# Kernel optimization log

Measured on AMD Instinct MI355X. Metric: run time of the kernel, lower is better.

The kernel has to match this reference:

```python
import jax, jax.numpy as jnp
import numpy as np

SUB_NO, T_NO, T_DATA, E_NO, I_NO, N_BASIS = 20, 200, 50000, 2000, 500, 20


def _make_cos_basis():
    x = np.arange(T_NO, dtype=np.float32)
    raw = 6.0 * np.log(x + 1.0)  # cos_scale=6, cos_shift=1
    basis = np.zeros((N_BASIS, T_NO), np.float32)
    for i in range(N_BASIS):
        phi = 0.5 * np.pi * i
        b = 0.5 * np.cos(raw - phi) + 0.5
        basis[i] = np.where((raw < phi - np.pi) | (raw > phi + np.pi), 0.0, b)
    return basis


def _make_tree():
    C = np.zeros((SUB_NO, SUB_NO), np.int32)
    for p in range(SUB_NO):
        for c in (2 * p + 1, 2 * p + 2):
            if c < SUB_NO:
                C[p, c] = 1
    return C


def _one_hot_assign(n_syn):
    C = np.zeros((SUB_NO, n_syn), np.int32)
    C[np.arange(n_syn) % SUB_NO, np.arange(n_syn)] = 1
    return C


def setup_inputs() -> dict:
    key = jax.random.key(0)
    ks = jax.random.split(key, 12)
    f32 = jnp.float32
    S_e = (jax.random.uniform(ks[0], (T_DATA, E_NO)) < 0.02).astype(f32)
    S_i = (jax.random.uniform(ks[1], (T_DATA, I_NO)) < 0.02).astype(f32)
    Z = (jax.random.uniform(ks[2], (T_DATA,)) < 0.05).astype(f32)
    return {
        "S_e": S_e, "S_i": S_i, "Z": Z,
        "C_den": jnp.asarray(_make_tree()),
        "C_syn_e": jnp.asarray(_one_hot_assign(E_NO)),
        "C_syn_i": jnp.asarray(_one_hot_assign(I_NO)),
        "cos_basis": jnp.asarray(_make_cos_basis()),
        "W_syn": jax.random.normal(ks[3], (SUB_NO, N_BASIS, 2), f32) * 0.1,
        "W_hist": jax.random.normal(ks[4], (N_BASIS,), f32) * 0.1,
        "W_sub": jnp.ones((SUB_NO,), f32) * 0.1,
        "W_spk": jnp.ones((1,), f32),
        "Tau_spk": jnp.ones((1,), f32) * 3.0,
        "V_o": jax.random.normal(ks[5], (1,), f32),
        "Theta": jax.random.normal(ks[6], (SUB_NO,), f32) * 0.1,
        "weight1": jax.random.normal(ks[7], (SUB_NO, 5), f32) * 0.1,
        "weight2": jax.random.normal(ks[8], (SUB_NO, 5, 5), f32) * 0.1,
        "weight3": jax.random.normal(ks[9], (SUB_NO, 5, 5), f32) * 0.1,
        "weight4": jax.random.normal(ks[10], (5, SUB_NO), f32) * 0.1,
    }


def reference(S_e, S_i, Z, C_den, C_syn_e, C_syn_i, cos_basis, W_syn, W_hist,
              W_sub, W_spk, Tau_spk, V_o, Theta, weight1, weight2, weight3, weight4):
    f32 = jnp.float32
    T = S_e.shape[0]
    sub_no = weight1.shape[0]
    T_no = cos_basis.shape[1]
    Cd = C_den.astype(f32)

    # synapse -> subunit projection
    syn_e = S_e @ C_syn_e.astype(f32).T  # [T, sub]
    syn_i = S_i @ C_syn_i.astype(f32).T

    e_kern = W_syn[:, :, 0] @ cos_basis  # [sub, T_no]
    i_kern = W_syn[:, :, 1] @ cos_basis

    def grouped_causal_conv(x, kern):
        # torch: pad T_no-1 zeros in front, grouped conv with flipped kernel (true causal conv)
        xp = jnp.pad(x, ((T_no - 1, 0), (0, 0))).T[None]  # [1, sub, T+T_no-1]
        k = kern[:, None, ::-1]  # [sub, 1, T_no]
        y = jax.lax.conv_general_dilated(xp, k, (1,), 'VALID',
                                         dimension_numbers=('NCH', 'OIH', 'NCH'),
                                         feature_group_count=x.shape[1])
        return y[0].T  # [T, sub]

    syn = grouped_causal_conv(syn_e, e_kern) + grouped_causal_conv(syn_i, i_kern)

    def causal_conv_lag1(z, kern):
        # torch: pad T_no zeros in front, valid conv with flipped kernel, drop last -> [T]
        zp = jnp.pad(z, (T_no, 0))[None, None]  # [1,1,T+T_no]
        k = kern[None, None, ::-1]
        y = jax.lax.conv_general_dilated(zp, k, (1,), 'VALID',
                                         dimension_numbers=('NCH', 'OIH', 'NCH'))
        return y[0, 0, :-1]

    hist_kern = W_hist @ cos_basis  # [T_no]
    hist_filt = causal_conv_lag1(Z, hist_kern)

    lrelu = jax.nn.leaky_relu  # negative_slope 0.01 matches torch default
    W_sub2 = W_sub ** 2

    def sub_mlp(s, x):
        h = lrelu(x[:, None] * weight1[s][None, :])  # [T,5]
        h = lrelu(h @ weight2[s])
        h = lrelu(h @ weight3[s])
        return h @ weight4[:, s]  # [T]

    # tree recurrence: children have higher index, processed last-to-first
    ns_out = jnp.zeros((T, sub_no), f32)
    for s in range(sub_no - 1):
        sub_idx = sub_no - 1 - s
        agg = ns_out @ (Cd[sub_idx] * W_sub2)  # equals gather-leaf weighted sum (0 if leaf)
        ns_in = lrelu(syn[:, sub_idx] + Theta[sub_idx] + agg)
        ns_out = ns_out.at[:, sub_idx].set(sub_mlp(sub_idx, ns_in))

    root_in = lrelu(hist_filt + syn[:, 0] + ns_out @ (Cd[0] * W_sub2) + Theta[0])
    final_Z = jax.nn.sigmoid(sub_mlp(0, root_in))

    t = jnp.arange(T_no, dtype=f32)
    t_tau = t / Tau_spk[0] ** 2
    spk_kern = t_tau * jnp.exp(-t_tau) * W_spk[0] ** 2
    final_V = causal_conv_lag1(Z, spk_kern) + V_o[0]

    out_filters = jnp.concatenate([e_kern, i_kern, hist_kern[None, :]], axis=0)
    return final_V, final_Z, out_filters
```

## Files before the change

### kernel.cpp

```cpp
#include <hip/hip_runtime.h>
#include <math.h>

#define T_DATA 50000
#define SUB_NO 20
#define T_NO 200
#define N_BASIS 20

#define WS_E    0
#define WS_I    1000000
#define WS_EKT  2000000
#define WS_IKT  2004000
#define WS_WSE  2008400
#define WS_HF   2008800

#define KA_RED_BLOCKS 977
#define KA_HIST_BLOCKS 196
#define KA_TOTAL (KA_RED_BLOCKS + 1 + KA_HIST_BLOCKS)

__device__ __forceinline__ float lrelu(float x) { return x > 0.f ? x : 0.01f * x; }

__global__ __launch_bounds__(256) void kA(const float* __restrict__ Se,
                                          const float* __restrict__ Si,
                                          const float* __restrict__ Z,
                                          const int* __restrict__ C_den,
                                          const float* __restrict__ cb,
                                          const float* __restrict__ W_syn,
                                          const float* __restrict__ W_hist,
                                          const float* __restrict__ W_sub,
                                          const float* __restrict__ W_spk,
                                          const float* __restrict__ Tau,
                                          const float* __restrict__ Vo,
                                          float* __restrict__ ws,
                                          float* __restrict__ out) {
    int tid = threadIdx.x;
    int bid = blockIdx.x;

    if (bid < KA_RED_BLOCKS) {
        int gid = bid * 256 + tid;
        if (gid >= T_DATA * 5) return;
        int t = gid / 5, sg = gid % 5;
        const float4* Se4 = (const float4*)Se;
        const float4* Si4 = (const float4*)Si;

        float4 a = make_float4(0.f, 0.f, 0.f, 0.f);
        int base_e = t * 500 + sg;
        #pragma unroll 10
        for (int g = 0; g < 100; g++) {
            float4 v = Se4[base_e + g * 5];
            a.x += v.x; a.y += v.y; a.z += v.z; a.w += v.w;
        }
        float4 b = make_float4(0.f, 0.f, 0.f, 0.f);
        int base_i = t * 125 + sg;
        #pragma unroll
        for (int g = 0; g < 25; g++) {
            float4 v = Si4[base_i + g * 5];
            b.x += v.x; b.y += v.y; b.z += v.z; b.w += v.w;
        }
        ((float4*)(ws + WS_E))[t * 5 + sg] = a;
        ((float4*)(ws + WS_I))[t * 5 + sg] = b;
        return;
    }

    if (bid == KA_RED_BLOCKS) {
        for (int j = tid; j < 4000; j += 256) {
            int s = j / 200, tau = j % 200;
            float se = 0.f, si = 0.f;
            #pragma unroll
            for (int b = 0; b < N_BASIS; b++) {
                float c = cb[b * 200 + tau];
                se += W_syn[(s * N_BASIS + b) * 2 + 0] * c;
                si += W_syn[(s * N_BASIS + b) * 2 + 1] * c;
            }
            ws[WS_EKT + tau * 20 + s] = se;
            ws[WS_IKT + tau * 20 + s] = si;
            out[2 * T_DATA + j] = se;
            out[2 * T_DATA + 4000 + j] = si;
        }
        for (int j = tid; j < 200; j += 256) {
            float h = 0.f;
            #pragma unroll
            for (int b = 0; b < N_BASIS; b++) h += W_hist[b] * cb[b * 200 + j];
            out[2 * T_DATA + 8000 + j] = h;
        }
        for (int j = tid; j < 400; j += 256) {
            int c = j % 20;
            ws[WS_WSE + j] = (float)C_den[j] * W_sub[c] * W_sub[c];
        }
        return;
    }

    __shared__ float z[456];
    __shared__ float2 hk[200];
    int t0 = (bid - KA_RED_BLOCKS - 1) * 256;
    for (int f = tid; f < 456; f += 256) {
        int u = t0 - 200 + f;
        z[f] = (u >= 0 && u < T_DATA) ? Z[u] : 0.f;
    }
    if (tid < 200) {
        float h = 0.f;
        #pragma unroll
        for (int b = 0; b < N_BASIS; b++) h += W_hist[b] * cb[b * 200 + tid];
        float tau2 = Tau[0] * Tau[0];
        float tt = (float)tid / tau2;
        float sk = tt * expf(-tt) * W_spk[0] * W_spk[0];
        hk[tid] = make_float2(h, sk);
    }
    __syncthreads();
    float ha = 0.f, sa = 0.f;
    #pragma unroll 4
    for (int tau = 0; tau < T_NO; tau++) {
        float zv = z[tid + 199 - tau];
        float2 hv = hk[tau];
        ha += zv * hv.x;
        sa += zv * hv.y;
    }
    int t = t0 + tid;
    if (t < T_DATA) {
        out[t] = sa + Vo[0];
        ws[WS_HF + t] = ha;
    }
}

__device__ __forceinline__ float sub_mlp(int s, float x,
                                         const float* __restrict__ w1,
                                         const float* __restrict__ w2,
                                         const float* __restrict__ w3,
                                         const float* __restrict__ w4) {
    float h1[5], h2[5], h3[5];
    #pragma unroll
    for (int k = 0; k < 5; k++) h1[k] = lrelu(x * w1[s * 5 + k]);
    #pragma unroll
    for (int j = 0; j < 5; j++) {
        float v = 0.f;
        #pragma unroll
        for (int k = 0; k < 5; k++) v += h1[k] * w2[s * 25 + k * 5 + j];
        h2[j] = lrelu(v);
    }
    #pragma unroll
    for (int j = 0; j < 5; j++) {
        float v = 0.f;
        #pragma unroll
        for (int k = 0; k < 5; k++) v += h2[k] * w3[s * 25 + k * 5 + j];
        h3[j] = lrelu(v);
    }
    float o = 0.f;
    #pragma unroll
    for (int k = 0; k < 5; k++) o += h3[k] * w4[k * 20 + s];
    return o;
}

#define KB_X 64
#define KB_T 256
#define KB_ROWS 455
#define KB_SRP 115
#define KB_THREADS 640

__global__ __launch_bounds__(KB_THREADS) void kB(const float* __restrict__ ws,
                                                 const float* __restrict__ Theta,
                                                 const float* __restrict__ w1,
                                                 const float* __restrict__ w2,
                                                 const float* __restrict__ w3,
                                                 const float* __restrict__ w4,
                                                 float* __restrict__ out) {
    __shared__ float4 tile[2 * 5 * 4 * KB_SRP];
    __shared__ float4 hkE[1000];
    __shared__ float4 hkI[1000];
    int x = threadIdx.x;
    int sg = __builtin_amdgcn_readfirstlane(threadIdx.y);
    int z  = __builtin_amdgcn_readfirstlane(threadIdx.z);
    int t0 = blockIdx.x * KB_T;
    int lin = x + 64 * sg + 320 * z;

    const float4* wsE4 = (const float4*)(ws + WS_E);
    const float4* wsI4 = (const float4*)(ws + WS_I);
    long gbase = (long)(t0 - 199) * 5;
    for (int f = lin; f < KB_ROWS * 5; f += KB_THREADS) {
        long g = gbase + f;
        int row = f / 5, gg = f % 5;
        int sub = row & 3, idx = row >> 2;
        float4 ve = make_float4(0.f, 0.f, 0.f, 0.f);
        float4 vi = ve;
        if (g >= 0 && g < (long)T_DATA * 5) {
            ve = wsE4[g];
            vi = wsI4[g];
        }
        tile[((0 * 5 + gg) * 4 + sub) * KB_SRP + idx] = ve;
        tile[((1 * 5 + gg) * 4 + sub) * KB_SRP + idx] = vi;
    }
    const float4* eK = (const float4*)(ws + WS_EKT);
    const float4* iK = (const float4*)(ws + WS_IKT);
    for (int f = lin; f < 1000; f += KB_THREADS) {
        hkE[f] = eK[f];
        hkI[f] = iK[f];
    }
    __syncthreads();

    const float4* te = &tile[(0 * 5 + sg) * 4 * KB_SRP];
    const float4* ti = &tile[(1 * 5 + sg) * 4 * KB_SRP];

    float4 we[4], wi[4], acc[4];
    #pragma unroll
    for (int j = 0; j < 4; j++) acc[j] = make_float4(0.f, 0.f, 0.f, 0.f);
    int idx0 = x + 50 - 25 * z;
    we[0] = te[0 * KB_SRP + idx0]; wi[0] = ti[0 * KB_SRP + idx0];
    we[1] = te[1 * KB_SRP + idx0]; wi[1] = ti[1 * KB_SRP + idx0];
    we[2] = te[2 * KB_SRP + idx0]; wi[2] = ti[2 * KB_SRP + idx0];

    int m0 = 25 * z;
    for (int mm = 0; mm < 25; mm++) {
        int m = m0 + mm;
        int idx = x + 49 - m;
        #pragma unroll
        for (int p = 0; p < 4; p++) {
            int tau = 4 * m + p;
            const int s0 = (3 - p) & 3;
            we[s0] = te[s0 * KB_SRP + idx];
            wi[s0] = ti[s0 * KB_SRP + idx];
            float4 ke = hkE[tau * 5 + sg];
            float4 ki = hkI[tau * 5 + sg];
            #pragma unroll
            for (int j = 0; j < 4; j++) {
                const int sl = (s0 + j) & 3;
                acc[j].x += we[sl].x * ke.x + wi[sl].x * ki.x;
                acc[j].y += we[sl].y * ke.y + wi[sl].y * ki.y;
                acc[j].z += we[sl].z * ke.z + wi[sl].z * ki.z;
                acc[j].w += we[sl].w * ke.w + wi[sl].w * ki.w;
            }
        }
    }

    __syncthreads();
    float4* accP = tile;
    #pragma unroll
    for (int j = 0; j < 4; j++) accP[((z * 20) + sg * 4 + j) * 64 + x] = acc[j];
    __syncthreads();

    if (lin >= 256) return;
    int w = lin >> 6, xr = lin & 63;
    int t = t0 + 4 * xr + w;
    if (t >= T_DATA) return;

    float acc20[20];
    #pragma unroll
    for (int g = 0; g < 5; g++) {
        float4 v0 = accP[(g * 4 + w) * 64 + xr];
        float4 v1 = accP[(20 + g * 4 + w) * 64 + xr];
        acc20[g * 4 + 0] = v0.x + v1.x; acc20[g * 4 + 1] = v0.y + v1.y;
        acc20[g * 4 + 2] = v0.z + v1.z; acc20[g * 4 + 3] = v0.w + v1.w;
    }
    const float* wse = ws + WS_WSE;
    float ns[20];
    #pragma unroll
    for (int s = 0; s < 20; s++) ns[s] = 0.f;
    #pragma unroll
    for (int si = 19; si >= 1; si--) {
        float ag = 0.f;
        #pragma unroll
        for (int c = 0; c < 20; c++) ag += wse[si * 20 + c] * ns[c];
        float xx = lrelu(acc20[si] + Theta[si] + ag);
        ns[si] = sub_mlp(si, xx, w1, w2, w3, w4);
    }
    float ag0 = 0.f;
    #pragma unroll
    for (int c = 0; c < 20; c++) ag0 += wse[c] * ns[c];
    float x0 = lrelu(ws[WS_HF + t] + acc20[0] + ag0 + Theta[0]);
    float zf = sub_mlp(0, x0, w1, w2, w3, w4);
    out[T_DATA + t] = 1.f / (1.f + expf(-zf));
}

extern "C" void kernel_launch(void* const* d_in, const int* in_sizes, int n_in,
                              void* d_out, int out_size, void* d_ws, size_t ws_size,
                              hipStream_t stream) {
    const float* S_e    = (const float*)d_in[0];
    const float* S_i    = (const float*)d_in[1];
    const float* Z      = (const float*)d_in[2];
    const int*   C_den  = (const int*)d_in[3];
    const float* cb     = (const float*)d_in[6];
    const float* W_syn  = (const float*)d_in[7];
    const float* W_hist = (const float*)d_in[8];
    const float* W_sub  = (const float*)d_in[9];
    const float* W_spk  = (const float*)d_in[10];
    const float* Tau    = (const float*)d_in[11];
    const float* V_o    = (const float*)d_in[12];
    const float* Theta  = (const float*)d_in[13];
    const float* w1     = (const float*)d_in[14];
    const float* w2     = (const float*)d_in[15];
    const float* w3     = (const float*)d_in[16];
    const float* w4     = (const float*)d_in[17];
    float* out = (float*)d_out;
    float* ws  = (float*)d_ws;

    kA<<<KA_TOTAL, 256, 0, stream>>>(S_e, S_i, Z, C_den, cb, W_syn, W_hist,
                                     W_sub, W_spk, Tau, V_o, ws, out);
    dim3 b3(KB_X, 5, 2);
    kB<<<(T_DATA + KB_T - 1) / KB_T, b3, 0, stream>>>(
        ws, Theta, w1, w2, w3, w4, out);
}
```

Before: 657.4 us.

## Restructure spike reduction for contiguous loads and read kernels from global in kB

The reduction phase of kA now runs 320 threads per block covering 64 time rows. Each thread reads a contiguous 100-float4 chunk of a row (25 for S_i) into five strided partial sums, and a shared-memory pass then combines the partials across the five thread groups into the same grouped output layout. This is meant to make the bandwidth-bound scan of S_e and S_i more cache-line friendly. In kB, the filter kernels are no longer staged in LDS and are read straight from global memory in the inner loop. That saves LDS and allows more blocks per CU, at the risk of more global or cache traffic in the hot loop.

```diff
diff --git a/kernel.cpp b/kernel.cpp
--- a/kernel.cpp
+++ b/kernel.cpp
@@ -13,56 +13,102 @@
 #define WS_WSE  2008400
 #define WS_HF   2008800
 
-#define KA_RED_BLOCKS 977
-#define KA_HIST_BLOCKS 196
+#define KA_THREADS 320
+#define KA_RED_BLOCKS 782
+#define KA_HIST_BLOCKS 157
 #define KA_TOTAL (KA_RED_BLOCKS + 1 + KA_HIST_BLOCKS)
 
 __device__ __forceinline__ float lrelu(float x) { return x > 0.f ? x : 0.01f * x; }
 
-__global__ __launch_bounds__(256) void kA(const float* __restrict__ Se,
-                                          const float* __restrict__ Si,
-                                          const float* __restrict__ Z,
-                                          const int* __restrict__ C_den,
-                                          const float* __restrict__ cb,
-                                          const float* __restrict__ W_syn,
-                                          const float* __restrict__ W_hist,
-                                          const float* __restrict__ W_sub,
-                                          const float* __restrict__ W_spk,
-                                          const float* __restrict__ Tau,
-                                          const float* __restrict__ Vo,
-                                          float* __restrict__ ws,
-                                          float* __restrict__ out) {
+__global__ __launch_bounds__(KA_THREADS) void kA(const float* __restrict__ Se,
+                                                 const float* __restrict__ Si,
+                                                 const float* __restrict__ Z,
+                                                 const int* __restrict__ C_den,
+                                                 const float* __restrict__ cb,
+                                                 const float* __restrict__ W_syn,
+                                                 const float* __restrict__ W_hist,
+                                                 const float* __restrict__ W_sub,
+                                                 const float* __restrict__ W_spk,
+                                                 const float* __restrict__ Tau,
+                                                 const float* __restrict__ Vo,
+                                                 float* __restrict__ ws,
+                                                 float* __restrict__ out) {
     int tid = threadIdx.x;
     int bid = blockIdx.x;
 
+    __shared__ float4 red[KA_THREADS * 5];
+    __shared__ float zsh[520];
+    __shared__ float2 hk[200];
+
     if (bid < KA_RED_BLOCKS) {
-        int gid = bid * 256 + tid;
-        if (gid >= T_DATA * 5) return;
-        int t = gid / 5, sg = gid % 5;
+        int r2 = tid / 5, sg = tid % 5;
+        int t = bid * 64 + r2;
+        bool valid = (t < T_DATA);
         const float4* Se4 = (const float4*)Se;
         const float4* Si4 = (const float4*)Si;
 
-        float4 a = make_float4(0.f, 0.f, 0.f, 0.f);
-        int base_e = t * 500 + sg;
-        #pragma unroll 10
-        for (int g = 0; g < 100; g++) {
-            float4 v = Se4[base_e + g * 5];
-            a.x += v.x; a.y += v.y; a.z += v.z; a.w += v.w;
-        }
-        float4 b = make_float4(0.f, 0.f, 0.f, 0.f);
-        int base_i = t * 125 + sg;
-        #pragma unroll
-        for (int g = 0; g < 25; g++) {
-            float4 v = Si4[base_i + g * 5];
-            b.x += v.x; b.y += v.y; b.z += v.z; b.w += v.w;
-        }
-        ((float4*)(ws + WS_E))[t * 5 + sg] = a;
-        ((float4*)(ws + WS_I))[t * 5 + sg] = b;
+        float4 aE[5], aI[5];
+        #pragma unroll
+        for (int r = 0; r < 5; r++) {
+            aE[r] = make_float4(0.f, 0.f, 0.f, 0.f);
+            aI[r] = aE[r];
+        }
+        if (valid) {
+            const float4* rowE = Se4 + (long)t * 500 + sg * 100;
+            #pragma unroll 2
+            for (int uu = 0; uu < 20; uu++) {
+                #pragma unroll
+                for (int r = 0; r < 5; r++) {
+                    float4 v = rowE[uu * 5 + r];
+                    aE[r].x += v.x; aE[r].y += v.y;
+                    aE[r].z += v.z; aE[r].w += v.w;
+                }
+            }
+            const float4* rowI = Si4 + (long)t * 125 + sg * 25;
+            #pragma unroll 2
+            for (int uu = 0; uu < 5; uu++) {
+                #pragma unroll
+                for (int r = 0; r < 5; r++) {
+                    float4 v = rowI[uu * 5 + r];
+                    aI[r].x += v.x; aI[r].y += v.y;
+                    aI[r].z += v.z; aI[r].w += v.w;
+                }
+            }
+        }
+        #pragma unroll
+        for (int r = 0; r < 5; r++) red[tid * 5 + r] = aE[r];
+        __syncthreads();
+        {
+            int rr = tid / 5, k = tid % 5;
+            float4 s = make_float4(0.f, 0.f, 0.f, 0.f);
+            #pragma unroll
+            for (int g = 0; g < 5; g++) {
+                float4 v = red[(rr * 5 + g) * 5 + k];
+                s.x += v.x; s.y += v.y; s.z += v.z; s.w += v.w;
+            }
+            if (t < T_DATA)
+                ((float4*)(ws + WS_E))[bid * KA_THREADS + tid] = s;
+        }
+        __syncthreads();
+        #pragma unroll
+        for (int r = 0; r < 5; r++) red[tid * 5 + r] = aI[r];
+        __syncthreads();
+        {
+            int rr = tid / 5, k = tid % 5;
+            float4 s = make_float4(0.f, 0.f, 0.f, 0.f);
+            #pragma unroll
+            for (int g = 0; g < 5; g++) {
+                float4 v = red[(rr * 5 + g) * 5 + k];
+                s.x += v.x; s.y += v.y; s.z += v.z; s.w += v.w;
+            }
+            if (t < T_DATA)
+                ((float4*)(ws + WS_I))[bid * KA_THREADS + tid] = s;
+        }
         return;
     }
 
     if (bid == KA_RED_BLOCKS) {
-        for (int j = tid; j < 4000; j += 256) {
+        for (int j = tid; j < 4000; j += KA_THREADS) {
             int s = j / 200, tau = j % 200;
             float se = 0.f, si = 0.f;
             #pragma unroll
@@ -76,25 +122,23 @@
             out[2 * T_DATA + j] = se;
             out[2 * T_DATA + 4000 + j] = si;
         }
-        for (int j = tid; j < 200; j += 256) {
+        for (int j = tid; j < 200; j += KA_THREADS) {
             float h = 0.f;
             #pragma unroll
             for (int b = 0; b < N_BASIS; b++) h += W_hist[b] * cb[b * 200 + j];
             out[2 * T_DATA + 8000 + j] = h;
         }
-        for (int j = tid; j < 400; j += 256) {
+        for (int j = tid; j < 400; j += KA_THREADS) {
             int c = j % 20;
             ws[WS_WSE + j] = (float)C_den[j] * W_sub[c] * W_sub[c];
         }
         return;
     }
 
-    __shared__ float z[456];
-    __shared__ float2 hk[200];
-    int t0 = (bid - KA_RED_BLOCKS - 1) * 256;
-    for (int f = tid; f < 456; f += 256) {
+    int t0 = (bid - KA_RED_BLOCKS - 1) * KA_THREADS;
+    for (int f = tid; f < 520; f += KA_THREADS) {
         int u = t0 - 200 + f;
-        z[f] = (u >= 0 && u < T_DATA) ? Z[u] : 0.f;
+        zsh[f] = (u >= 0 && u < T_DATA) ? Z[u] : 0.f;
     }
     if (tid < 200) {
         float h = 0.f;
@@ -109,7 +153,7 @@
     float ha = 0.f, sa = 0.f;
     #pragma unroll 4
     for (int tau = 0; tau < T_NO; tau++) {
-        float zv = z[tid + 199 - tau];
+        float zv = zsh[tid + 199 - tau];
         float2 hv = hk[tau];
         ha += zv * hv.x;
         sa += zv * hv.y;
@@ -163,8 +207,6 @@
                                                  const float* __restrict__ w4,
                                                  float* __restrict__ out) {
     __shared__ float4 tile[2 * 5 * 4 * KB_SRP];
-    __shared__ float4 hkE[1000];
-    __shared__ float4 hkI[1000];
     int x = threadIdx.x;
     int sg = __builtin_amdgcn_readfirstlane(threadIdx.y);
     int z  = __builtin_amdgcn_readfirstlane(threadIdx.z);
@@ -187,14 +229,10 @@
         tile[((0 * 5 + gg) * 4 + sub) * KB_SRP + idx] = ve;
         tile[((1 * 5 + gg) * 4 + sub) * KB_SRP + idx] = vi;
     }
+    __syncthreads();
+
     const float4* eK = (const float4*)(ws + WS_EKT);
     const float4* iK = (const float4*)(ws + WS_IKT);
-    for (int f = lin; f < 1000; f += KB_THREADS) {
-        hkE[f] = eK[f];
-        hkI[f] = iK[f];
-    }
-    __syncthreads();
-
     const float4* te = &tile[(0 * 5 + sg) * 4 * KB_SRP];
     const float4* ti = &tile[(1 * 5 + sg) * 4 * KB_SRP];
 
@@ -216,8 +254,8 @@
             const int s0 = (3 - p) & 3;
             we[s0] = te[s0 * KB_SRP + idx];
             wi[s0] = ti[s0 * KB_SRP + idx];
-            float4 ke = hkE[tau * 5 + sg];
-            float4 ki = hkI[tau * 5 + sg];
+            float4 ke = eK[tau * 5 + sg];
+            float4 ki = iK[tau * 5 + sg];
             #pragma unroll
             for (int j = 0; j < 4; j++) {
                 const int sl = (s0 + j) & 3;
@@ -290,8 +328,9 @@
     float* out = (float*)d_out;
     float* ws  = (float*)d_ws;
 
-    kA<<<KA_TOTAL, 256, 0, stream>>>(S_e, S_i, Z, C_den, cb, W_syn, W_hist,
-                                     W_sub, W_spk, Tau, V_o, ws, out);
+    kA<<<KA_TOTAL, KA_THREADS, 0, stream>>>(S_e, S_i, Z, C_den, cb, W_syn,
+                                            W_hist, W_sub, W_spk, Tau, V_o,
+                                            ws, out);
     dim3 b3(KB_X, 5, 2);
     kB<<<(T_DATA + KB_T - 1) / KB_T, b3, 0, stream>>>(
         ws, Theta, w1, w2, w3, w4, out);
```

New measurement: 695.3 us. 5.8% more time.

## Fuse both kernels into one cooperative persistent kernel with grid sync

Applied to the files above, without the earlier changes.

Merges the reduction/filter kernel and the convolution+tree kernel into a single cooperative launch of 256 blocks. A grid-wide barrier separates the two phases, removing one kernel launch and its gap. The history convolution now reads Z straight from global memory instead of staging it in shared memory. The convolution kernels are also read from global memory instead of being copied into LDS. Risks include grid-sync overhead, and the reduction phase now running on only 256 blocks, which may give less memory parallelism than the earlier 977 blocks.

```diff
diff --git a/kernel.cpp b/kernel.cpp
--- a/kernel.cpp
+++ b/kernel.cpp
@@ -1,8 +1,10 @@
 #include <hip/hip_runtime.h>
+#include <hip/hip_cooperative_groups.h>
 #include <math.h>
 
+namespace cg = cooperative_groups;
+
 #define T_DATA 50000
-#define SUB_NO 20
 #define T_NO 200
 #define N_BASIS 20
 
@@ -13,113 +15,16 @@
 #define WS_WSE  2008400
 #define WS_HF   2008800
 
-#define KA_RED_BLOCKS 977
-#define KA_HIST_BLOCKS 196
-#define KA_TOTAL (KA_RED_BLOCKS + 1 + KA_HIST_BLOCKS)
+#define NBLK 256
+#define NTHR 640
+#define GSTRIDE (NBLK * NTHR)
+
+#define KB_T 256
+#define KB_ROWS 455
+#define KB_SRP 115
+#define KB_CHUNKS 196
 
 __device__ __forceinline__ float lrelu(float x) { return x > 0.f ? x : 0.01f * x; }
-
-__global__ __launch_bounds__(256) void kA(const float* __restrict__ Se,
-                                          const float* __restrict__ Si,
-                                          const float* __restrict__ Z,
-                                          const int* __restrict__ C_den,
-                                          const float* __restrict__ cb,
-                                          const float* __restrict__ W_syn,
-                                          const float* __restrict__ W_hist,
-                                          const float* __restrict__ W_sub,
-                                          const float* __restrict__ W_spk,
-                                          const float* __restrict__ Tau,
-                                          const float* __restrict__ Vo,
-                                          float* __restrict__ ws,
-                                          float* __restrict__ out) {
-    int tid = threadIdx.x;
-    int bid = blockIdx.x;
-
-    if (bid < KA_RED_BLOCKS) {
-        int gid = bid * 256 + tid;
-        if (gid >= T_DATA * 5) return;
-        int t = gid / 5, sg = gid % 5;
-        const float4* Se4 = (const float4*)Se;
-        const float4* Si4 = (const float4*)Si;
-
-        float4 a = make_float4(0.f, 0.f, 0.f, 0.f);
-        int base_e = t * 500 + sg;
-        #pragma unroll 10
-        for (int g = 0; g < 100; g++) {
-            float4 v = Se4[base_e + g * 5];
-            a.x += v.x; a.y += v.y; a.z += v.z; a.w += v.w;
-        }
-        float4 b = make_float4(0.f, 0.f, 0.f, 0.f);
-        int base_i = t * 125 + sg;
-        #pragma unroll
-        for (int g = 0; g < 25; g++) {
-            float4 v = Si4[base_i + g * 5];
-            b.x += v.x; b.y += v.y; b.z += v.z; b.w += v.w;
-        }
-        ((float4*)(ws + WS_E))[t * 5 + sg] = a;
-        ((float4*)(ws + WS_I))[t * 5 + sg] = b;
-        return;
-    }
-
-    if (bid == KA_RED_BLOCKS) {
-        for (int j = tid; j < 4000; j += 256) {
-            int s = j / 200, tau = j % 200;
-            float se = 0.f, si = 0.f;
-            #pragma unroll
-            for (int b = 0; b < N_BASIS; b++) {
-                float c = cb[b * 200 + tau];
-                se += W_syn[(s * N_BASIS + b) * 2 + 0] * c;
-                si += W_syn[(s * N_BASIS + b) * 2 + 1] * c;
-            }
-            ws[WS_EKT + tau * 20 + s] = se;
-            ws[WS_IKT + tau * 20 + s] = si;
-            out[2 * T_DATA + j] = se;
-            out[2 * T_DATA + 4000 + j] = si;
-        }
-        for (int j = tid; j < 200; j += 256) {
-            float h = 0.f;
-            #pragma unroll
-            for (int b = 0; b < N_BASIS; b++) h += W_hist[b] * cb[b * 200 + j];
-            out[2 * T_DATA + 8000 + j] = h;
-        }
-        for (int j = tid; j < 400; j += 256) {
-            int c = j % 20;
-            ws[WS_WSE + j] = (float)C_den[j] * W_sub[c] * W_sub[c];
-        }
-        return;
-    }
-
-    __shared__ float z[456];
-    __shared__ float2 hk[200];
-    int t0 = (bid - KA_RED_BLOCKS - 1) * 256;
-    for (int f = tid; f < 456; f += 256) {
-        int u = t0 - 200 + f;
-        z[f] = (u >= 0 && u < T_DATA) ? Z[u] : 0.f;
-    }
-    if (tid < 200) {
-        float h = 0.f;
-        #pragma unroll
-        for (int b = 0; b < N_BASIS; b++) h += W_hist[b] * cb[b * 200 + tid];
-        float tau2 = Tau[0] * Tau[0];
-        float tt = (float)tid / tau2;
-        float sk = tt * expf(-tt) * W_spk[0] * W_spk[0];
-        hk[tid] = make_float2(h, sk);
-    }
-    __syncthreads();
-    float ha = 0.f, sa = 0.f;
-    #pragma unroll 4
-    for (int tau = 0; tau < T_NO; tau++) {
-        float zv = z[tid + 199 - tau];
-        float2 hv = hk[tau];
-        ha += zv * hv.x;
-        sa += zv * hv.y;
-    }
-    int t = t0 + tid;
-    if (t < T_DATA) {
-        out[t] = sa + Vo[0];
-        ws[WS_HF + t] = ha;
-    }
-}
 
 __device__ __forceinline__ float sub_mlp(int s, float x,
                                          const float* __restrict__ w1,
@@ -149,32 +54,118 @@
     return o;
 }
 
-#define KB_X 64
-#define KB_T 256
-#define KB_ROWS 455
-#define KB_SRP 115
-#define KB_THREADS 640
-
-__global__ __launch_bounds__(KB_THREADS) void kB(const float* __restrict__ ws,
-                                                 const float* __restrict__ Theta,
-                                                 const float* __restrict__ w1,
-                                                 const float* __restrict__ w2,
-                                                 const float* __restrict__ w3,
-                                                 const float* __restrict__ w4,
-                                                 float* __restrict__ out) {
-    __shared__ float4 tile[2 * 5 * 4 * KB_SRP];
-    __shared__ float4 hkE[1000];
-    __shared__ float4 hkI[1000];
-    int x = threadIdx.x;
-    int sg = __builtin_amdgcn_readfirstlane(threadIdx.y);
-    int z  = __builtin_amdgcn_readfirstlane(threadIdx.z);
-    int t0 = blockIdx.x * KB_T;
-    int lin = x + 64 * sg + 320 * z;
+__global__ __launch_bounds__(NTHR) void kFused(
+        const float* __restrict__ Se, const float* __restrict__ Si,
+        const float* __restrict__ Z, const int* __restrict__ C_den,
+        const float* __restrict__ cb, const float* __restrict__ W_syn,
+        const float* __restrict__ W_hist, const float* __restrict__ W_sub,
+        const float* __restrict__ W_spk, const float* __restrict__ Tau,
+        const float* __restrict__ Vo, const float* __restrict__ Theta,
+        const float* __restrict__ w1, const float* __restrict__ w2,
+        const float* __restrict__ w3, const float* __restrict__ w4,
+        float* __restrict__ ws, float* __restrict__ out) {
+    __shared__ float4 smem4[2 * 5 * 4 * KB_SRP];
+    int tid = threadIdx.x;
+    int bid = blockIdx.x;
+
+    {
+        const float4* Se4 = (const float4*)Se;
+        const float4* Si4 = (const float4*)Si;
+        float4* wsE4 = (float4*)(ws + WS_E);
+        float4* wsI4 = (float4*)(ws + WS_I);
+        for (int g = bid * NTHR + tid; g < T_DATA * 5; g += GSTRIDE) {
+            int t = g / 5, s5 = g % 5;
+            float4 a = make_float4(0.f, 0.f, 0.f, 0.f);
+            int base_e = t * 500 + s5;
+            #pragma unroll 10
+            for (int k = 0; k < 100; k++) {
+                float4 v = Se4[base_e + k * 5];
+                a.x += v.x; a.y += v.y; a.z += v.z; a.w += v.w;
+            }
+            float4 b = make_float4(0.f, 0.f, 0.f, 0.f);
+            int base_i = t * 125 + s5;
+            #pragma unroll
+            for (int k = 0; k < 25; k++) {
+                float4 v = Si4[base_i + k * 5];
+                b.x += v.x; b.y += v.y; b.z += v.z; b.w += v.w;
+            }
+            wsE4[g] = a;
+            wsI4[g] = b;
+        }
+    }
+
+    if (bid < 79) {
+        float2* hk = (float2*)smem4;
+        if (tid < 200) {
+            float h = 0.f;
+            #pragma unroll
+            for (int b = 0; b < N_BASIS; b++) h += W_hist[b] * cb[b * 200 + tid];
+            float tau2 = Tau[0] * Tau[0];
+            float tt = (float)tid / tau2;
+            float sk = tt * expf(-tt) * W_spk[0] * W_spk[0];
+            hk[tid] = make_float2(h, sk);
+        }
+        __syncthreads();
+        int t = bid * NTHR + tid;
+        if (t < T_DATA) {
+            float ha = 0.f, sa = 0.f;
+            #pragma unroll 4
+            for (int tau = 0; tau < T_NO; tau++) {
+                int u = t - 1 - tau;
+                float zv = (u >= 0) ? Z[u] : 0.f;
+                float2 hv = hk[tau];
+                ha += zv * hv.x;
+                sa += zv * hv.y;
+            }
+            out[t] = sa + Vo[0];
+            ws[WS_HF + t] = ha;
+        }
+    }
+
+    if (bid == NBLK - 1) {
+        for (int j = tid; j < 4000; j += NTHR) {
+            int s = j / 200, tau = j % 200;
+            float se = 0.f, si = 0.f;
+            #pragma unroll
+            for (int b = 0; b < N_BASIS; b++) {
+                float c = cb[b * 200 + tau];
+                se += W_syn[(s * N_BASIS + b) * 2 + 0] * c;
+                si += W_syn[(s * N_BASIS + b) * 2 + 1] * c;
+            }
+            ws[WS_EKT + tau * 20 + s] = se;
+            ws[WS_IKT + tau * 20 + s] = si;
+            out[2 * T_DATA + j] = se;
+            out[2 * T_DATA + 4000 + j] = si;
+        }
+        for (int j = tid; j < 200; j += NTHR) {
+            float h = 0.f;
+            #pragma unroll
+            for (int b = 0; b < N_BASIS; b++) h += W_hist[b] * cb[b * 200 + j];
+            out[2 * T_DATA + 8000 + j] = h;
+        }
+        for (int j = tid; j < 400; j += NTHR) {
+            int c = j % 20;
+            ws[WS_WSE + j] = (float)C_den[j] * W_sub[c] * W_sub[c];
+        }
+    }
+
+    __threadfence();
+    cg::this_grid().sync();
+
+    if (bid >= KB_CHUNKS) return;
+
+    float4* tile = smem4;
+    int x = tid & 63;
+    int wv = tid >> 6;
+    int sg = __builtin_amdgcn_readfirstlane(wv % 5);
+    int z  = __builtin_amdgcn_readfirstlane(wv / 5);
+    int t0 = bid * KB_T;
+    int lin = tid;
 
     const float4* wsE4 = (const float4*)(ws + WS_E);
     const float4* wsI4 = (const float4*)(ws + WS_I);
     long gbase = (long)(t0 - 199) * 5;
-    for (int f = lin; f < KB_ROWS * 5; f += KB_THREADS) {
+    for (int f = lin; f < KB_ROWS * 5; f += NTHR) {
         long g = gbase + f;
         int row = f / 5, gg = f % 5;
         int sub = row & 3, idx = row >> 2;
@@ -187,14 +178,10 @@
         tile[((0 * 5 + gg) * 4 + sub) * KB_SRP + idx] = ve;
         tile[((1 * 5 + gg) * 4 + sub) * KB_SRP + idx] = vi;
     }
+    __syncthreads();
+
     const float4* eK = (const float4*)(ws + WS_EKT);
     const float4* iK = (const float4*)(ws + WS_IKT);
-    for (int f = lin; f < 1000; f += KB_THREADS) {
-        hkE[f] = eK[f];
-        hkI[f] = iK[f];
-    }
-    __syncthreads();
-
     const float4* te = &tile[(0 * 5 + sg) * 4 * KB_SRP];
     const float4* ti = &tile[(1 * 5 + sg) * 4 * KB_SRP];
 
@@ -216,8 +203,8 @@
             const int s0 = (3 - p) & 3;
             we[s0] = te[s0 * KB_SRP + idx];
             wi[s0] = ti[s0 * KB_SRP + idx];
-            float4 ke = hkE[tau * 5 + sg];
-            float4 ki = hkI[tau * 5 + sg];
+            float4 ke = eK[tau * 5 + sg];
+            float4 ki = iK[tau * 5 + sg];
             #pragma unroll
             for (int j = 0; j < 4; j++) {
                 const int sl = (s0 + j) & 3;
@@ -290,9 +277,13 @@
     float* out = (float*)d_out;
     float* ws  = (float*)d_ws;
 
-    kA<<<KA_TOTAL, 256, 0, stream>>>(S_e, S_i, Z, C_den, cb, W_syn, W_hist,
-                                     W_sub, W_spk, Tau, V_o, ws, out);
-    dim3 b3(KB_X, 5, 2);
-    kB<<<(T_DATA + KB_T - 1) / KB_T, b3, 0, stream>>>(
-        ws, Theta, w1, w2, w3, w4, out);
+    void* args[] = {
+        (void*)&S_e, (void*)&S_i, (void*)&Z, (void*)&C_den, (void*)&cb,
+        (void*)&W_syn, (void*)&W_hist, (void*)&W_sub, (void*)&W_spk,
+        (void*)&Tau, (void*)&V_o, (void*)&Theta,
+        (void*)&w1, (void*)&w2, (void*)&w3, (void*)&w4,
+        (void*)&ws, (void*)&out
+    };
+    hipLaunchCooperativeKernel((void*)kFused, dim3(NBLK), dim3(NTHR),
+                               args, 0, stream);
 }
```

After: 820.6 us. 24.8% more time.

## Coalesce synaptic row reduction via LDS, read kernels from global in kB

Applied to the files above, without the earlier changes.

The synapse-count reduction in kA now gives each 20-thread group one time row, so consecutive lanes read contiguous float4s, then reduces the partials through shared memory. The kernel-build block moves to the last block index. kB no longer stages the e/i temporal kernels in LDS and instead loads them directly from global (wave-uniform, so they can use scalar or cached loads). This frees LDS for occupancy but adds global loads inside the inner loop.

```diff
diff --git a/kernel.cpp b/kernel.cpp
--- a/kernel.cpp
+++ b/kernel.cpp
@@ -2,7 +2,6 @@
 #include <math.h>
 
 #define T_DATA 50000
-#define SUB_NO 20
 #define T_NO 200
 #define N_BASIS 20
 
@@ -13,9 +12,10 @@
 #define WS_WSE  2008400
 #define WS_HF   2008800
 
-#define KA_RED_BLOCKS 977
+#define KA_ROWS_PB 12
+#define KA_RED_BLOCKS 4167
 #define KA_HIST_BLOCKS 196
-#define KA_TOTAL (KA_RED_BLOCKS + 1 + KA_HIST_BLOCKS)
+#define KA_TOTAL (KA_RED_BLOCKS + KA_HIST_BLOCKS + 1)
 
 __device__ __forceinline__ float lrelu(float x) { return x > 0.f ? x : 0.01f * x; }
 
@@ -36,88 +36,115 @@
     int bid = blockIdx.x;
 
     if (bid < KA_RED_BLOCKS) {
-        int gid = bid * 256 + tid;
-        if (gid >= T_DATA * 5) return;
-        int t = gid / 5, sg = gid % 5;
+        __shared__ float4 ldsE[KA_ROWS_PB * 20];
+        __shared__ float4 ldsI[KA_ROWS_PB * 20];
+        int t_loc = tid / 20, sg = tid % 20;
+        int t = bid * KA_ROWS_PB + t_loc;
+        bool act = (tid < KA_ROWS_PB * 20) && (t < T_DATA);
         const float4* Se4 = (const float4*)Se;
         const float4* Si4 = (const float4*)Si;
 
-        float4 a = make_float4(0.f, 0.f, 0.f, 0.f);
-        int base_e = t * 500 + sg;
-        #pragma unroll 10
-        for (int g = 0; g < 100; g++) {
-            float4 v = Se4[base_e + g * 5];
-            a.x += v.x; a.y += v.y; a.z += v.z; a.w += v.w;
-        }
-        float4 b = make_float4(0.f, 0.f, 0.f, 0.f);
-        int base_i = t * 125 + sg;
-        #pragma unroll
-        for (int g = 0; g < 25; g++) {
-            float4 v = Si4[base_i + g * 5];
-            b.x += v.x; b.y += v.y; b.z += v.z; b.w += v.w;
-        }
-        ((float4*)(ws + WS_E))[t * 5 + sg] = a;
-        ((float4*)(ws + WS_I))[t * 5 + sg] = b;
+        float4 aE = make_float4(0.f, 0.f, 0.f, 0.f);
+        float4 aI = make_float4(0.f, 0.f, 0.f, 0.f);
+        if (act) {
+            const float4* rowE = Se4 + (long)t * 500;
+            #pragma unroll
+            for (int k = 0; k < 25; k++) {
+                float4 v = rowE[sg + 20 * k];
+                aE.x += v.x; aE.y += v.y; aE.z += v.z; aE.w += v.w;
+            }
+            const float4* rowI = Si4 + (long)t * 125;
+            #pragma unroll
+            for (int k = 0; k < 7; k++) {
+                int f = sg + 20 * k;
+                if (f < 125) {
+                    float4 v = rowI[f];
+                    aI.x += v.x; aI.y += v.y; aI.z += v.z; aI.w += v.w;
+                }
+            }
+        }
+        if (tid < KA_ROWS_PB * 20) {
+            ldsE[tid] = aE;
+            ldsI[tid] = aI;
+        }
+        __syncthreads();
+        if (tid < KA_ROWS_PB * 5) {
+            int tl = tid / 5, r = tid % 5;
+            float4 sE = make_float4(0.f, 0.f, 0.f, 0.f);
+            float4 sI = make_float4(0.f, 0.f, 0.f, 0.f);
+            #pragma unroll
+            for (int m = 0; m < 4; m++) {
+                float4 vE = ldsE[tl * 20 + r + 5 * m];
+                float4 vI = ldsI[tl * 20 + r + 5 * m];
+                sE.x += vE.x; sE.y += vE.y; sE.z += vE.z; sE.w += vE.w;
+                sI.x += vI.x; sI.y += vI.y; sI.z += vI.z; sI.w += vI.w;
+            }
+            int tt = bid * KA_ROWS_PB + tl;
+            if (tt < T_DATA) {
+                ((float4*)(ws + WS_E))[tt * 5 + r] = sE;
+                ((float4*)(ws + WS_I))[tt * 5 + r] = sI;
+            }
+        }
         return;
     }
 
-    if (bid == KA_RED_BLOCKS) {
-        for (int j = tid; j < 4000; j += 256) {
-            int s = j / 200, tau = j % 200;
-            float se = 0.f, si = 0.f;
-            #pragma unroll
-            for (int b = 0; b < N_BASIS; b++) {
-                float c = cb[b * 200 + tau];
-                se += W_syn[(s * N_BASIS + b) * 2 + 0] * c;
-                si += W_syn[(s * N_BASIS + b) * 2 + 1] * c;
-            }
-            ws[WS_EKT + tau * 20 + s] = se;
-            ws[WS_IKT + tau * 20 + s] = si;
-            out[2 * T_DATA + j] = se;
-            out[2 * T_DATA + 4000 + j] = si;
-        }
-        for (int j = tid; j < 200; j += 256) {
+    if (bid < KA_RED_BLOCKS + KA_HIST_BLOCKS) {
+        __shared__ float z[456];
+        __shared__ float2 hk[200];
+        int t0 = (bid - KA_RED_BLOCKS) * 256;
+        for (int f = tid; f < 456; f += 256) {
+            int u = t0 - 200 + f;
+            z[f] = (u >= 0 && u < T_DATA) ? Z[u] : 0.f;
+        }
+        if (tid < 200) {
             float h = 0.f;
             #pragma unroll
-            for (int b = 0; b < N_BASIS; b++) h += W_hist[b] * cb[b * 200 + j];
-            out[2 * T_DATA + 8000 + j] = h;
-        }
-        for (int j = tid; j < 400; j += 256) {
-            int c = j % 20;
-            ws[WS_WSE + j] = (float)C_den[j] * W_sub[c] * W_sub[c];
+            for (int b = 0; b < N_BASIS; b++) h += W_hist[b] * cb[b * 200 + tid];
+            float tau2 = Tau[0] * Tau[0];
+            float tt = (float)tid / tau2;
+            float sk = tt * expf(-tt) * W_spk[0] * W_spk[0];
+            hk[tid] = make_float2(h, sk);
+        }
+        __syncthreads();
+        float ha = 0.f, sa = 0.f;
+        #pragma unroll 4
+        for (int tau = 0; tau < T_NO; tau++) {
+            float zv = z[tid + 199 - tau];
+            float2 hv = hk[tau];
+            ha += zv * hv.x;
+            sa += zv * hv.y;
+        }
+        int t = t0 + tid;
+        if (t < T_DATA) {
+            out[t] = sa + Vo[0];
+            ws[WS_HF + t] = ha;
         }
         return;
     }
 
-    __shared__ float z[456];
-    __shared__ float2 hk[200];
-    int t0 = (bid - KA_RED_BLOCKS - 1) * 256;
-    for (int f = tid; f < 456; f += 256) {
-        int u = t0 - 200 + f;
-        z[f] = (u >= 0 && u < T_DATA) ? Z[u] : 0.f;
-    }
-    if (tid < 200) {
+    for (int j = tid; j < 4000; j += 256) {
+        int s = j / 200, tau = j % 200;
+        float se = 0.f, si = 0.f;
+        #pragma unroll
+        for (int b = 0; b < N_BASIS; b++) {
+            float c = cb[b * 200 + tau];
+            se += W_syn[(s * N_BASIS + b) * 2 + 0] * c;
+            si += W_syn[(s * N_BASIS + b) * 2 + 1] * c;
+        }
+        ws[WS_EKT + tau * 20 + s] = se;
+        ws[WS_IKT + tau * 20 + s] = si;
+        out[2 * T_DATA + j] = se;
+        out[2 * T_DATA + 4000 + j] = si;
+    }
+    for (int j = tid; j < 200; j += 256) {
         float h = 0.f;
         #pragma unroll
-        for (int b = 0; b < N_BASIS; b++) h += W_hist[b] * cb[b * 200 + tid];
-        float tau2 = Tau[0] * Tau[0];
-        float tt = (float)tid / tau2;
-        float sk = tt * expf(-tt) * W_spk[0] * W_spk[0];
-        hk[tid] = make_float2(h, sk);
-    }
-    __syncthreads();
-    float ha = 0.f, sa = 0.f;
-    #pragma unroll 4
-    for (int tau = 0; tau < T_NO; tau++) {
-        float zv = z[tid + 199 - tau];
-        float2 hv = hk[tau];
-        ha += zv * hv.x;
-        sa += zv * hv.y;
-    }
-    int t = t0 + tid;
-    if (t < T_DATA) {
-        out[t] = sa + Vo[0];
-        ws[WS_HF + t] = ha;
+        for (int b = 0; b < N_BASIS; b++) h += W_hist[b] * cb[b * 200 + j];
+        out[2 * T_DATA + 8000 + j] = h;
+    }
+    for (int j = tid; j < 400; j += 256) {
+        int c = j % 20;
+        ws[WS_WSE + j] = (float)C_den[j] * W_sub[c] * W_sub[c];
     }
 }
 
@@ -163,8 +190,6 @@
                                                  const float* __restrict__ w4,
                                                  float* __restrict__ out) {
     __shared__ float4 tile[2 * 5 * 4 * KB_SRP];
-    __shared__ float4 hkE[1000];
-    __shared__ float4 hkI[1000];
     int x = threadIdx.x;
     int sg = __builtin_amdgcn_readfirstlane(threadIdx.y);
     int z  = __builtin_amdgcn_readfirstlane(threadIdx.z);
@@ -187,14 +212,10 @@
         tile[((0 * 5 + gg) * 4 + sub) * KB_SRP + idx] = ve;
         tile[((1 * 5 + gg) * 4 + sub) * KB_SRP + idx] = vi;
     }
+    __syncthreads();
+
     const float4* eK = (const float4*)(ws + WS_EKT);
     const float4* iK = (const float4*)(ws + WS_IKT);
-    for (int f = lin; f < 1000; f += KB_THREADS) {
-        hkE[f] = eK[f];
-        hkI[f] = iK[f];
-    }
-    __syncthreads();
-
     const float4* te = &tile[(0 * 5 + sg) * 4 * KB_SRP];
     const float4* ti = &tile[(1 * 5 + sg) * 4 * KB_SRP];
 
@@ -216,8 +237,8 @@
             const int s0 = (3 - p) & 3;
             we[s0] = te[s0 * KB_SRP + idx];
             wi[s0] = ti[s0 * KB_SRP + idx];
-            float4 ke = hkE[tau * 5 + sg];
-            float4 ki = hkI[tau * 5 + sg];
+            float4 ke = eK[tau * 5 + sg];
+            float4 ki = iK[tau * 5 + sg];
             #pragma unroll
             for (int j = 0; j < 4; j++) {
                 const int sl = (s0 + j) & 3;
```

After: 663.1 us. About the same (+0.9%).
